# Kernel optimization log

Hardware: AMD Instinct MI355X
Metric: run time of the kernel (lower is better)

Reference implementation:

```python
import jax, jax.numpy as jnp
import numpy as np

DIM = 1024
S_SIZE = 512
M_SIZE = 4096
L_SIZE = 8192
MERGE_THRESHOLD = 0.98
L_ALPHA = 0.1
K_PROMOTE = max(1, S_SIZE // 4)  # torch: min(len(candidates), max(1, s_size//4)); candidates >> s_size here


def _l2norm(x, axis=-1):
    # F.normalize(p=2) with eps clamp
    return x / jnp.maximum(jnp.linalg.norm(x, axis=axis, keepdims=True), 1e-12)


def _update(processed_tokens, s_memory, m_memory, l_memory, m_utility, l_utility, wq, bq, wk, bk, s_ptr):
    cand = processed_tokens.reshape(-1, DIM)
    # --- S tier: scatter top-k-norm candidates into ring buffer (vectorized; K<=S so slots distinct) ---
    norms = jnp.linalg.norm(cand, axis=1)
    _, top_idx = jax.lax.top_k(norms, K_PROMOTE)
    pos = (s_ptr + jnp.arange(K_PROMOTE)) % S_SIZE
    s_mem = s_memory.at[pos].set(cand[top_idx])
    s_ptr_new = (s_ptr + K_PROMOTE) % S_SIZE
    # --- promotion attention (1 head, only attn weights used): pick best short-term slot ---
    q = l_memory.mean(axis=0) @ wq.T + bq                      # [dim]
    kproj = s_mem @ wk.T + bk                                  # [S, dim]
    attn = jax.nn.softmax(kproj @ q / jnp.sqrt(jnp.asarray(DIM, cand.dtype)))
    best_s_idx = jnp.argmax(attn)
    candidate = s_mem[best_s_idx]                              # [dim]

    # --- M tier: promote / merge / replace ---
    def not_full(mm, mu):
        ridx = jnp.argmin(mu)
        return mm.at[ridx].set(candidate), mu.at[ridx].set(mu.mean() + 1e-5)

    def full(mm, mu):
        mm_norm = _l2norm(mm)
        sims = mm_norm @ _l2norm(candidate)                    # [M]
        msi = jnp.argmax(sims)
        sim_cand = sims[msi]

        def merge_with_candidate(mm, mu):
            merged = _l2norm((mm[msi] + candidate) / 2.0)
            return mm.at[msi].set(merged), mu.at[msi].set((mu[msi] + mu.mean()) / 2.0)

        def try_internal_merge(mm, mu):
            # most redundant pair: strict lower triangle of cosine sim matrix
            sim_mat = mm_norm @ mm_norm.T                      # [M, M]
            sim_mat = jnp.where(jnp.triu(jnp.ones((M_SIZE, M_SIZE), bool)), -1.0, sim_mat)
            flat = jnp.argmax(sim_mat)
            internal_sim = sim_mat.reshape(-1)[flat]
            idx1, idx2 = flat // M_SIZE, flat % M_SIZE

            def do_pair_merge(mm, mu):
                merged = _l2norm((mm[idx1] + mm[idx2]) / 2.0)
                mm2 = mm.at[idx1].set(merged).at[idx2].set(candidate)
                mu1 = mu.at[idx1].set((mu[idx1] + mu[idx2]) / 2.0)
                mu2 = mu1.at[idx2].set(mu1.mean() + 1e-5)      # torch recomputes mean after idx1 write
                return mm2, mu2

            def replace_weakest(mm, mu):
                li = jnp.argmin(mu)
                stronger = jnp.linalg.norm(candidate) > jnp.linalg.norm(mm[li])
                mm2 = jnp.where(stronger, mm.at[li].set(candidate), mm)
                mu2 = jnp.where(stronger, mu.at[li].set(mu.mean() + 1e-5), mu)
                return mm2, mu2

            return jax.lax.cond(internal_sim > MERGE_THRESHOLD, do_pair_merge, replace_weakest, mm, mu)

        return jax.lax.cond(sim_cand > MERGE_THRESHOLD, merge_with_candidate, try_internal_merge, mm, mu)

    is_m_full = ~jnp.any(m_utility == 0)
    m_mem, m_util = jax.lax.cond(is_m_full, full, not_full, m_memory, m_utility)
    # --- L tier: consolidate most-used M slot into least-used L slot ---
    mi = jnp.argmax(m_util)
    lj = jnp.argmin(l_utility)
    consolidated = (1.0 - L_ALPHA) * l_memory[lj] + L_ALPHA * m_mem[mi]
    l_mem = l_memory.at[lj].set(consolidated)
    l_util = l_utility.at[lj].set(l_utility.mean())            # mean of pre-write values
    return s_mem, m_mem, l_mem, m_util, l_util, s_ptr_new


def setup_inputs() -> dict:
    key = jax.random.key(0)
    ks = jax.random.split(key, 10)
    scale = 1.0 / np.sqrt(DIM)
    return {
        "processed_tokens": jax.random.normal(ks[0], (4, 4096, DIM), jnp.float32),
        "s_memory": jax.random.normal(ks[1], (S_SIZE, DIM), jnp.float32),
        "m_memory": jax.random.normal(ks[2], (M_SIZE, DIM), jnp.float32),
        "l_memory": jax.random.normal(ks[3], (L_SIZE, DIM), jnp.float32),
        "m_utility": jax.random.uniform(ks[4], (M_SIZE,), jnp.float32) + 0.01,  # >0 -> 'm full' branch
        "l_utility": jax.random.uniform(ks[5], (L_SIZE,), jnp.float32) + 0.01,
        "wq": jax.random.normal(ks[6], (DIM, DIM), jnp.float32) * scale,
        "bq": jnp.zeros((DIM,), jnp.float32),
        "wk": jax.random.normal(ks[7], (DIM, DIM), jnp.float32) * scale,
        "bk": jnp.zeros((DIM,), jnp.float32),
        "s_ptr": 0,
    }


def reference(processed_tokens, s_memory, m_memory, l_memory, m_utility, l_utility, wq, bq, wk, bk, s_ptr):
    return _update(processed_tokens, s_memory, m_memory, l_memory, m_utility, l_utility, wq, bq, wk, bk, s_ptr)
```

## Files before the change

kernel.cpp:

```cpp
#include <hip/hip_runtime.h>

#define DIMV 1024
#define SSZ 512
#define MSZ 4096
#define LSZ 8192
#define KPROM 128
#define NCAND 16384
#define NPAIR 528

typedef __attribute__((ext_vector_type(4))) float f32x4;
typedef __attribute__((ext_vector_type(4))) unsigned int u32x4;
typedef __attribute__((ext_vector_type(4))) unsigned short u16x4;
typedef __attribute__((ext_vector_type(8))) __bf16 bf16x8;

#define OUT_S 0ull
#define OUT_M 524288ull
#define OUT_L 4718592ull
#define OUT_MU 13107200ull
#define OUT_LU 13111296ull
#define OUT_SPTR 13119488ull

#define SCROWS 2304
#define SC_BF16 0ull
#define SC_NORMS 2097152ull
#define SC_TOPIDX 2113536ull
#define SC_LPART 2113664ull
#define SC_RVP 2244736ull
#define SC_LOGITS 2261120ull
#define SC_BEST 2261632ull
#define SC_MNORM 2261636ull
#define SC_SIMS 2265732ull
#define SC_PPV 2269828ull
#define SC_PPI 2270356ull

__device__ __forceinline__ float wave_sum(float v) {
#pragma unroll
  for (int o = 32; o > 0; o >>= 1) v += __shfl_down(v, o, 64);
  return v;
}
__device__ __forceinline__ void wave_maxidx(float& v, int& i) {
#pragma unroll
  for (int o = 32; o > 0; o >>= 1) {
    float ov = __shfl_down(v, o, 64);
    int oi = __shfl_down(i, o, 64);
    if (ov > v || (ov == v && oi < i)) { v = ov; i = oi; }
  }
}
__device__ __forceinline__ void wave_minidx(float& v, int& i) {
#pragma unroll
  for (int o = 32; o > 0; o >>= 1) {
    float ov = __shfl_down(v, o, 64);
    int oi = __shfl_down(i, o, 64);
    if (ov < v || (ov == v && oi < i)) { v = ov; i = oi; }
  }
}
__device__ __forceinline__ unsigned short f2bf(float x) {
  unsigned u = __float_as_uint(x);
  return (unsigned short)((u + 0x7FFFu + ((u >> 16) & 1u)) >> 16);
}
__device__ __forceinline__ void gload16(const unsigned short* g, unsigned short* l) {
  __builtin_amdgcn_global_load_lds((const __attribute__((address_space(1))) unsigned int*)(g),
                                   (__attribute__((address_space(3))) unsigned int*)(l), 16, 0, 0);
}

__global__ void kA(const float* __restrict__ cand, const float* __restrict__ l_memory,
                   const float* __restrict__ m, float* __restrict__ norms,
                   float* __restrict__ lpart, unsigned short* __restrict__ mb,
                   float* __restrict__ mnorm, float* __restrict__ out_m,
                   float* __restrict__ out_l, int* __restrict__ cnt) {
  int b = blockIdx.x, t = threadIdx.x, lane = t & 63, w = t >> 6;
  if (b == 0 && t == 0) cnt[0] = 0;
  if (b < 128) {
    int r0 = b * 64;
    const f32x4* base = (const f32x4*)l_memory + (size_t)r0 * 256;
    f32x4* dst = (f32x4*)out_l + (size_t)r0 * 256;
    bool wr = (r0 >= SCROWS);
    f32x4 a0 = {0.f, 0.f, 0.f, 0.f}, a1 = a0, a2 = a0, a3 = a0;
#pragma unroll 2
    for (int r = 0; r < 64; r += 4) {
      f32x4 v0 = base[(r + 0) * 256 + t];
      f32x4 v1 = base[(r + 1) * 256 + t];
      f32x4 v2 = base[(r + 2) * 256 + t];
      f32x4 v3 = base[(r + 3) * 256 + t];
      if (wr) {
        dst[(r + 0) * 256 + t] = v0;
        dst[(r + 1) * 256 + t] = v1;
        dst[(r + 2) * 256 + t] = v2;
        dst[(r + 3) * 256 + t] = v3;
      }
      a0 += v0; a1 += v1; a2 += v2; a3 += v3;
    }
    f32x4 a = (a0 + a1) + (a2 + a3);
    ((f32x4*)(lpart + (size_t)b * DIMV))[t] = a;
  } else if (b < 384) {
    int r0 = (b - 128) * 16 + w * 4;
    const f32x4* base4 = (const f32x4*)(m + (size_t)r0 * DIMV);
    u16x4* mb4 = (u16x4*)(mb + (size_t)r0 * DIMV);
    f32x4* om4 = (f32x4*)(out_m + (size_t)r0 * DIMV);
    float s0 = 0.f, s1 = 0.f, s2 = 0.f, s3 = 0.f;
#pragma unroll
    for (int k = 0; k < 16; ++k) {
      int i = k * 64 + lane;
      f32x4 v = base4[i];
      float d = v.x * v.x + v.y * v.y + v.z * v.z + v.w * v.w;
      if (k < 4) s0 += d;
      else if (k < 8) s1 += d;
      else if (k < 12) s2 += d;
      else s3 += d;
      u16x4 h;
      h.x = f2bf(v.x); h.y = f2bf(v.y); h.z = f2bf(v.z); h.w = f2bf(v.w);
      mb4[i] = h;
      om4[i] = v;
    }
    f32x4 sv = {s0, s1, s2, s3};
#pragma unroll
    for (int o = 32; o > 0; o >>= 1) {
      sv.x += __shfl_down(sv.x, o, 64);
      sv.y += __shfl_down(sv.y, o, 64);
      sv.z += __shfl_down(sv.z, o, 64);
      sv.w += __shfl_down(sv.w, o, 64);
    }
    if (lane == 0) {
      f32x4 o4 = {sqrtf(sv.x), sqrtf(sv.y), sqrtf(sv.z), sqrtf(sv.w)};
      *((f32x4*)(mnorm + r0)) = o4;
    }
  } else {
    int r0 = (b - 384) * 16 + w * 4;
    const f32x4* base4 = (const f32x4*)(cand + (size_t)r0 * DIMV);
    float s0 = 0.f, s1 = 0.f, s2 = 0.f, s3 = 0.f;
#pragma unroll
    for (int k = 0; k < 16; ++k) {
      f32x4 v = base4[k * 64 + lane];
      float d = v.x * v.x + v.y * v.y + v.z * v.z + v.w * v.w;
      if (k < 4) s0 += d;
      else if (k < 8) s1 += d;
      else if (k < 12) s2 += d;
      else s3 += d;
    }
    f32x4 sv = {s0, s1, s2, s3};
#pragma unroll
    for (int o = 32; o > 0; o >>= 1) {
      sv.x += __shfl_down(sv.x, o, 64);
      sv.y += __shfl_down(sv.y, o, 64);
      sv.z += __shfl_down(sv.z, o, 64);
      sv.w += __shfl_down(sv.w, o, 64);
    }
    if (lane == 0) {
      f32x4 o4 = {sqrtf(sv.x), sqrtf(sv.y), sqrtf(sv.z), sqrtf(sv.w)};
      *((f32x4*)(norms + r0)) = o4;
    }
  }
}

__device__ int scan_excl_1024(int v, int* sh, int* total) {
  int t = threadIdx.x;
  sh[t] = v;
  __syncthreads();
  for (int o = 1; o < 1024; o <<= 1) {
    int x = (t >= o) ? sh[t - o] : 0;
    __syncthreads();
    sh[t] += x;
    __syncthreads();
  }
  int incl = sh[t];
  *total = sh[1023];
  __syncthreads();
  return incl - v;
}

__global__ void kT(const float* __restrict__ norms, int* __restrict__ topidx) {
  int t = threadIdx.x;
  __shared__ int sh[1024];
  __shared__ int hist[256];
  __shared__ unsigned s_selkey[KPROM];
  __shared__ int s_selidx[KPROM];
  __shared__ int s_digit, s_sub;
  unsigned key[16];
  {
    const u32x4* np = (const u32x4*)norms;
    u32x4 k0 = np[t * 4 + 0], k1 = np[t * 4 + 1], k2 = np[t * 4 + 2], k3 = np[t * 4 + 3];
    key[0] = k0.x; key[1] = k0.y; key[2] = k0.z; key[3] = k0.w;
    key[4] = k1.x; key[5] = k1.y; key[6] = k1.z; key[7] = k1.w;
    key[8] = k2.x; key[9] = k2.y; key[10] = k2.z; key[11] = k2.w;
    key[12] = k3.x; key[13] = k3.y; key[14] = k3.z; key[15] = k3.w;
  }

  unsigned prefix = 0, himask = 0;
  int remaining = KPROM;
  for (int p = 24; p >= 0; p -= 8) {
    if (t < 256) hist[t] = 0;
    __syncthreads();
#pragma unroll
    for (int j = 0; j < 16; ++j)
      if ((key[j] & himask) == prefix) atomicAdd(&hist[(key[j] >> p) & 255], 1);
    __syncthreads();
    if (t < 256) sh[t] = hist[t];
    __syncthreads();
    for (int o = 1; o < 256; o <<= 1) {
      int x = (t < 256 && t + o < 256) ? sh[t + o] : 0;
      __syncthreads();
      if (t < 256) sh[t] += x;
      __syncthreads();
    }
    if (t < 256) {
      int sfex = (t < 255) ? sh[t + 1] : 0;
      if (sfex < remaining && remaining <= sh[t]) { s_digit = t; s_sub = sfex; }
    }
    __syncthreads();
    prefix |= ((unsigned)s_digit) << p;
    remaining -= s_sub;
    himask |= (0xFFu << p);
    __syncthreads();
  }
  unsigned T = prefix;

  int cgt = 0, ceq = 0;
#pragma unroll
  for (int j = 0; j < 16; ++j) { cgt += (key[j] > T); ceq += (key[j] == T); }
  int total_gt, total_eq;
  int sgt = scan_excl_1024(cgt, sh, &total_gt);
  int seq = scan_excl_1024(ceq, sh, &total_eq);
  int need_eq = KPROM - total_gt;
  int g = sgt, e = seq;
#pragma unroll
  for (int j = 0; j < 16; ++j) {
    if (key[j] > T) { s_selkey[g] = key[j]; s_selidx[g] = t * 16 + j; ++g; }
    else if (key[j] == T) {
      if (e < need_eq) { s_selkey[total_gt + e] = key[j]; s_selidx[total_gt + e] = t * 16 + j; }
      ++e;
    }
  }
  __syncthreads();
  if (t < KPROM) {
    unsigned mk = s_selkey[t];
    int mi = s_selidx[t];
    int rank = 0;
    for (int q2 = 0; q2 < KPROM; ++q2) {
      unsigned qk = s_selkey[q2];
      int qi = s_selidx[q2];
      rank += (qk > mk || (qk == mk && qi < mi)) ? 1 : 0;
    }
    topidx[rank] = mi;
  }
}

__global__ void kBC(const float* __restrict__ cand, const float* __restrict__ s_memory,
                    const int* __restrict__ topidx, const int* __restrict__ s_ptr,
                    const float* __restrict__ wq, const float* __restrict__ bq,
                    const float* __restrict__ wk, const float* __restrict__ lpart,
                    float* __restrict__ rvpart, float* __restrict__ out_s,
                    float* __restrict__ out_sptr) {
  __shared__ float lmean_s[1024];
  __shared__ float qs[64];
  int b = blockIdx.x, t = threadIdx.x, lane = t & 63, w = t >> 6;
  if (b < 128) {
    int sp = s_ptr[0];
    if (b == 0 && t == 0) out_sptr[0] = (float)((sp + KPROM) % SSZ);
#pragma unroll
    for (int k = 0; k < 4; ++k) {
      int row = b * 4 + k;
      int ki = (row - sp + SSZ) & (SSZ - 1);
      const float* src =
          (ki < KPROM) ? (cand + (size_t)topidx[ki] * DIMV) : (s_memory + (size_t)row * DIMV);
      ((f32x4*)(out_s + (size_t)row * DIMV))[t] = ((const f32x4*)src)[t];
    }
    return;
  }
  int qb = b - 128, d0 = qb * 64;
  {
    f32x4 acc = {0.f, 0.f, 0.f, 0.f};
    for (int p = 0; p < 128; ++p) acc += ((const f32x4*)(lpart + (size_t)p * DIMV))[t];
    *(f32x4*)&lmean_s[t * 4] = acc * (1.f / 8192.f);
  }
  __syncthreads();
  for (int i = 0; i < 16; ++i) {
    int d = d0 + w * 16 + i;
    const f32x4* row = (const f32x4*)(wq + (size_t)d * DIMV);
    float s = 0.f;
#pragma unroll
    for (int c = 0; c < 4; ++c) {
      f32x4 a = row[c * 64 + lane];
      f32x4 bb = *(const f32x4*)&lmean_s[(c * 64 + lane) * 4];
      s += a.x * bb.x + a.y * bb.y + a.z * bb.z + a.w * bb.w;
    }
    s = wave_sum(s);
    if (lane == 0) qs[w * 16 + i] = s + bq[d];
  }
  __syncthreads();
  {
    f32x4 a = {0.f, 0.f, 0.f, 0.f};
    for (int r = 0; r < 64; ++r) {
      f32x4 v = ((const f32x4*)(wk + (size_t)(d0 + r) * DIMV))[t];
      a += v * qs[r];
    }
    ((f32x4*)(rvpart + (size_t)qb * DIMV))[t] = a;
  }
}

__global__ void kDE(const float* __restrict__ out_s, const float* __restrict__ rvpart,
                    float* __restrict__ logits, int* __restrict__ best,
                    float* __restrict__ cnorm, int* __restrict__ cnt) {
  __shared__ float rvs[1024];
  __shared__ float swv[4];
  __shared__ int swi[4];
  __shared__ int s_last;
  int b = blockIdx.x, t = threadIdx.x, lane = t & 63, w = t >> 6;
  {
    f32x4 acc = {0.f, 0.f, 0.f, 0.f};
#pragma unroll
    for (int p = 0; p < 16; ++p) acc += ((const f32x4*)(rvpart + (size_t)p * DIMV))[t];
    *(f32x4*)&rvs[t * 4] = acc;
  }
  __syncthreads();
  {
    int row = b * 4 + w;
    const f32x4* a4 = (const f32x4*)(out_s + (size_t)row * DIMV);
    float s = 0.f;
#pragma unroll
    for (int c = 0; c < 4; ++c) {
      f32x4 x = a4[c * 64 + lane];
      f32x4 y = *(const f32x4*)&rvs[(c * 64 + lane) * 4];
      s += x.x * y.x + x.y * y.y + x.z * y.z + x.w * y.w;
    }
    s = wave_sum(s);
    if (lane == 0) logits[row] = s;
  }
  __threadfence();
  __syncthreads();
  if (t == 0) {
    int a = __hip_atomic_fetch_add(cnt, 1, __ATOMIC_ACQ_REL, __HIP_MEMORY_SCOPE_AGENT);
    s_last = (a == 127) ? 1 : 0;
  }
  __syncthreads();
  if (!s_last) return;
  __threadfence();
  {
    float v0 = logits[t], v1 = logits[t + 256];
    float bv;
    int bidx;
    if (v1 > v0) { bv = v1; bidx = t + 256; } else { bv = v0; bidx = t; }
    wave_maxidx(bv, bidx);
    if (lane == 0) { swv[w] = bv; swi[w] = bidx; }
    __syncthreads();
    if (t == 0) {
      float a = swv[0]; int ai = swi[0];
      for (int i = 1; i < 4; ++i)
        if (swv[i] > a || (swv[i] == a && swi[i] < ai)) { a = swv[i]; ai = swi[i]; }
      best[0] = ai;
      cnt[0] = 0;
    }
    __syncthreads();
    int bi = best[0];
    f32x4 c4 = ((const f32x4*)(out_s + (size_t)bi * DIMV))[t];
    float s = c4.x * c4.x + c4.y * c4.y + c4.z * c4.z + c4.w * c4.w;
    s = wave_sum(s);
    __syncthreads();
    if (lane == 0) swv[w] = s;
    __syncthreads();
    if (t == 0) cnorm[0] = sqrtf(swv[0] + swv[1] + swv[2] + swv[3]);
  }
}

__global__ __launch_bounds__(256, 3) void kG(const unsigned short* __restrict__ mb,
                                             const float* __restrict__ mnorm,
                                             const float* __restrict__ m,
                                             const float* __restrict__ out_s,
                                             const int* __restrict__ best,
                                             const float* __restrict__ cnorm,
                                             float* __restrict__ pv, int* __restrict__ pidx,
                                             float* __restrict__ sims) {
  int b = blockIdx.x, t = threadIdx.x, lane = t & 63, w = t >> 6;
  if (b >= NPAIR) {
    int row = (b - NPAIR) * 4 + w;
    const f32x4* mp = (const f32x4*)(m + (size_t)row * DIMV);
    const f32x4* cp = (const f32x4*)(out_s + (size_t)best[0] * DIMV);
    float sd = 0.f;
#pragma unroll
    for (int c = 0; c < 4; ++c) {
      int i = c * 64 + lane;
      f32x4 v = mp[i], u = cp[i];
      sd += v.x * u.x + v.y * u.y + v.z * u.z + v.w * u.w;
    }
    sd = wave_sum(sd);
    if (lane == 0) sims[row] = sd / (fmaxf(mnorm[row], 1e-12f) * fmaxf(cnorm[0], 1e-12f));
    return;
  }
  __shared__ unsigned short Ash[128 * 64];
  __shared__ unsigned short Bsh[128 * 64];
  __shared__ float spv[4];
  __shared__ int spi[4];

  int bs = (b & 7) * 66 + (b >> 3);
  int bi = (int)((sqrtf(8.f * (float)bs + 1.f) - 1.f) * 0.5f);
  while (bi * (bi + 1) / 2 > bs) --bi;
  while ((bi + 1) * (bi + 2) / 2 <= bs) ++bi;
  int bj = bs - bi * (bi + 1) / 2;
  int rowA0 = bi * 128, rowB0 = bj * 128;

  int wr = w >> 1, wc = w & 1;
  int rl = lane & 15, kq4 = lane >> 4;
  int swz = rl & 7;
  int subrow = lane >> 3, gg = lane & 7;
  int gsw = (gg ^ subrow) << 3;

  f32x4 acc[4][4];
  f32x4 z = {0.f, 0.f, 0.f, 0.f};
#pragma unroll
  for (int ti = 0; ti < 4; ++ti)
#pragma unroll
    for (int tj = 0; tj < 4; ++tj) acc[ti][tj] = z;

  for (int kc = 0; kc < DIMV; kc += 64) {
#pragma unroll
    for (int jj = 0; jj < 4; ++jj) {
      int rsub = w * 32 + jj * 8 + subrow;
      gload16(mb + (size_t)(rowA0 + rsub) * DIMV + kc + gsw, Ash + (w * 4 + jj) * 512);
      gload16(mb + (size_t)(rowB0 + rsub) * DIMV + kc + gsw, Bsh + (w * 4 + jj) * 512);
    }
    __syncthreads();
#pragma unroll
    for (int ks = 0; ks < 2; ++ks) {
      int co = (((ks * 4 + kq4) ^ swz) << 3);
      bf16x8 af[4], bfv[4];
#pragma unroll
      for (int ti = 0; ti < 4; ++ti)
        af[ti] = *(const bf16x8*)(Ash + (wr * 64 + ti * 16 + rl) * 64 + co);
#pragma unroll
      for (int tj = 0; tj < 4; ++tj)
        bfv[tj] = *(const bf16x8*)(Bsh + (wc * 64 + tj * 16 + rl) * 64 + co);
#pragma unroll
      for (int ti = 0; ti < 4; ++ti)
#pragma unroll
        for (int tj = 0; tj < 4; ++tj)
          acc[ti][tj] = __builtin_amdgcn_mfma_f32_16x16x32_bf16(af[ti], bfv[tj], acc[ti][tj], 0, 0, 0);
    }
    __syncthreads();
  }

  float ni[16], nj4[4];
#pragma unroll
  for (int ti = 0; ti < 4; ++ti)
#pragma unroll
    for (int r = 0; r < 4; ++r)
      ni[ti * 4 + r] = fmaxf(mnorm[rowA0 + wr * 64 + ti * 16 + kq4 * 4 + r], 1e-12f);
#pragma unroll
  for (int tj = 0; tj < 4; ++tj)
    nj4[tj] = fmaxf(mnorm[rowB0 + wc * 64 + tj * 16 + rl], 1e-12f);

  float bv = -3.402823466e38f;
  int bidx = 0x7FFFFFFF;
#pragma unroll
  for (int ti = 0; ti < 4; ++ti)
#pragma unroll
    for (int tj = 0; tj < 4; ++tj)
#pragma unroll
      for (int r = 0; r < 4; ++r) {
        int gi = rowA0 + wr * 64 + ti * 16 + kq4 * 4 + r;
        int gj = rowB0 + wc * 64 + tj * 16 + rl;
        if (gi > gj) {
          float s = acc[ti][tj][r] / (ni[ti * 4 + r] * nj4[tj]);
          int fi = gi * MSZ + gj;
          if (s > bv || (s == bv && fi < bidx)) { bv = s; bidx = fi; }
        }
      }
  wave_maxidx(bv, bidx);
  if (lane == 0) { spv[w] = bv; spi[w] = bidx; }
  __syncthreads();
  if (t == 0) {
    float a = spv[0]; int ai = spi[0];
    for (int i = 1; i < 4; ++i)
      if (spv[i] > a || (spv[i] == a && spi[i] < ai)) { a = spv[i]; ai = spi[i]; }
    pv[b] = a;
    pidx[b] = ai;
  }
}

__global__ void kH(const float* __restrict__ pv, const int* __restrict__ pidx,
                   const float* __restrict__ sims, const float* __restrict__ mu,
                   const float* __restrict__ mnorm, const float* __restrict__ cnorm,
                   const int* __restrict__ best, const float* __restrict__ lu,
                   const float* __restrict__ m, const float* __restrict__ l_memory,
                   const float* __restrict__ out_s, float* __restrict__ out_mu,
                   float* __restrict__ out_lu, float* __restrict__ out_m,
                   float* __restrict__ out_l, int* __restrict__ ws) {
  __shared__ float swv[16];
  __shared__ int swi[16];
  __shared__ float ssum[16];
  __shared__ int szf[16];
  __shared__ float s_res[2];
  __shared__ int s_resi[2];
  __shared__ int s_branch, s_i1, s_i2, s_lj, s_best, s_mi;
  __shared__ float s_u1, s_u2, s_lmean, s_nrm;
  int t = threadIdx.x, lane = t & 63, w = t >> 6;

  float bv = -3.402823466e38f;
  int bidx = 0x7FFFFFFF;
  for (int i = t; i < NPAIR; i += 1024) {
    float v = pv[i];
    int fi = pidx[i];
    if (v > bv || (v == bv && fi < bidx)) { bv = v; bidx = fi; }
  }
  wave_maxidx(bv, bidx);
  if (lane == 0) { swv[w] = bv; swi[w] = bidx; }
  __syncthreads();
  if (t == 0) {
    float a = swv[0]; int ai = swi[0];
    for (int i = 1; i < 16; ++i)
      if (swv[i] > a || (swv[i] == a && swi[i] < ai)) { a = swv[i]; ai = swi[i]; }
    s_res[0] = a; s_resi[0] = ai;
  }
  __syncthreads();

  bv = -3.402823466e38f;
  bidx = 0x7FFFFFFF;
#pragma unroll
  for (int j = 0; j < 4; ++j) {
    int i = t * 4 + j;
    float v = sims[i];
    if (v > bv) { bv = v; bidx = i; }
  }
  wave_maxidx(bv, bidx);
  if (lane == 0) { swv[w] = bv; swi[w] = bidx; }
  __syncthreads();
  if (t == 0) {
    float a = swv[0]; int ai = swi[0];
    for (int i = 1; i < 16; ++i)
      if (swv[i] > a || (swv[i] == a && swi[i] < ai)) { a = swv[i]; ai = swi[i]; }
    s_res[1] = a; s_resi[1] = ai;
  }
  __syncthreads();

  float muv[4];
  float sum = 0.f, mnv = 3.402823466e38f;
  int mni = 0x7FFFFFFF, zf = 0;
#pragma unroll
  for (int j = 0; j < 4; ++j) {
    int i = t * 4 + j;
    float v = mu[i];
    muv[j] = v;
    sum += v;
    if (v < mnv) { mnv = v; mni = i; }
    if (v == 0.f) zf = 1;
  }
  sum = wave_sum(sum);
  wave_minidx(mnv, mni);
#pragma unroll
  for (int o = 32; o > 0; o >>= 1) zf |= __shfl_down(zf, o, 64);
  if (lane == 0) { ssum[w] = sum; swv[w] = mnv; swi[w] = mni; szf[w] = zf; }
  __syncthreads();
  if (t == 0) {
    float muSum = 0.f;
    int anyz = 0;
    float a = swv[0]; int li = swi[0];
    for (int i = 0; i < 16; ++i) {
      muSum += ssum[i];
      anyz |= szf[i];
      if (i > 0 && (swv[i] < a || (swv[i] == a && swi[i] < li))) { a = swv[i]; li = swi[i]; }
    }
    float muMean = muSum / 4096.f;
    float internal_sim = s_res[0];
    int iflat = s_resi[0];
    float sim_cand = s_res[1];
    int msi = s_resi[1];
    int branch, i1 = -1, i2 = -1;
    float u1 = 0.f, u2 = 0.f;
    if (anyz) {
      branch = 0; i1 = li; u1 = muMean + 1e-5f;
    } else if (sim_cand > 0.98f) {
      branch = 1; i1 = msi; u1 = (mu[msi] + muMean) * 0.5f;
    } else if (internal_sim > 0.98f) {
      branch = 2; i1 = iflat / MSZ; i2 = iflat - (iflat / MSZ) * MSZ;
      float o1 = mu[i1], o2 = mu[i2];
      u1 = (o1 + o2) * 0.5f;
      u2 = (muSum - o1 + u1) / 4096.f + 1e-5f;
    } else {
      if (cnorm[0] > mnorm[li]) { branch = 0; i1 = li; u1 = muMean + 1e-5f; }
      else branch = 4;
    }
    s_branch = branch; s_i1 = i1; s_i2 = i2; s_u1 = u1; s_u2 = u2;
    s_best = best[0];
    ws[2] = branch; ws[3] = i1; ws[4] = i2; ws[5] = best[0];
  }
  __syncthreads();

  int branch = s_branch, i1 = s_i1, i2 = s_i2;
  float u1 = s_u1, u2 = s_u2;
  bv = -3.402823466e38f;
  bidx = 0x7FFFFFFF;
#pragma unroll
  for (int j = 0; j < 4; ++j) {
    int i = t * 4 + j;
    float v = muv[j];
    if (branch != 4 && i == i1) v = u1;
    if (branch == 2 && i == i2) v = u2;
    out_mu[i] = v;
    if (v > bv) { bv = v; bidx = i; }
  }
  wave_maxidx(bv, bidx);
  __syncthreads();
  if (lane == 0) { swv[w] = bv; swi[w] = bidx; }
  __syncthreads();
  if (t == 0) {
    float a = swv[0]; int ai = swi[0];
    for (int i = 1; i < 16; ++i)
      if (swv[i] > a || (swv[i] == a && swi[i] < ai)) { a = swv[i]; ai = swi[i]; }
    ws[1] = ai;
    s_mi = ai;
  }

  float luv[8];
  sum = 0.f; mnv = 3.402823466e38f; mni = 0x7FFFFFFF;
#pragma unroll
  for (int j = 0; j < 8; ++j) {
    int i = t * 8 + j;
    float v = lu[i];
    luv[j] = v;
    sum += v;
    if (v < mnv) { mnv = v; mni = i; }
  }
  sum = wave_sum(sum);
  wave_minidx(mnv, mni);
  __syncthreads();
  if (lane == 0) { swv[w] = mnv; swi[w] = mni; ssum[w] = sum; }
  __syncthreads();
  if (t == 0) {
    float a = swv[0]; int ai = swi[0];
    float ls = 0.f;
    for (int i = 0; i < 16; ++i) {
      ls += ssum[i];
      if (i > 0 && (swv[i] < a || (swv[i] == a && swi[i] < ai))) { a = swv[i]; ai = swi[i]; }
    }
    s_lj = ai;
    s_lmean = ls / 8192.f;
    ws[0] = ai;
  }
  __syncthreads();
  {
    int lj = s_lj;
    float lmv = s_lmean;
#pragma unroll
    for (int j = 0; j < 8; ++j) {
      int i = t * 8 + j;
      out_lu[i] = (i == lj) ? lmv : luv[j];
    }
  }
  __syncthreads();

  int fbest = s_best, fmi = s_mi, flj = s_lj;
  const f32x4* csrc = (const f32x4*)(out_s + (size_t)fbest * DIMV);
  {
    f32x4 v = {0.f, 0.f, 0.f, 0.f};
    float ssv = 0.f;
    if (t < 256 && branch != 4 && branch != 0) {
      f32x4 a = ((const f32x4*)(m + (size_t)i1 * DIMV))[t];
      f32x4 bb = (branch == 1) ? csrc[t] : ((const f32x4*)(m + (size_t)i2 * DIMV))[t];
      v = (a + bb) * 0.5f;
      ssv = v.x * v.x + v.y * v.y + v.z * v.z + v.w * v.w;
    }
    ssv = wave_sum(ssv);
    __syncthreads();
    if (lane == 0) ssum[w] = ssv;
    __syncthreads();
    if (t == 0) {
      float s2 = 0.f;
      for (int i = 0; i < 16; ++i) s2 += ssum[i];
      s_nrm = fmaxf(sqrtf(s2), 1e-12f);
    }
    __syncthreads();
    if (t < 256 && branch != 4) {
      f32x4* dst = (f32x4*)(out_m + (size_t)i1 * DIMV);
      dst[t] = (branch == 0) ? csrc[t] : (v / s_nrm);
      if (branch == 2) ((f32x4*)(out_m + (size_t)i2 * DIMV))[t] = csrc[t];
    }
  }
  __syncthreads();

  {
    int mode = 0;
    if ((branch == 0 && fmi == i1) || (branch == 2 && fmi == i2)) mode = 1;
    else if (branch == 1 && fmi == i1) mode = 2;
    else if (branch == 2 && fmi == i1) mode = 3;
    f32x4 vm = {0.f, 0.f, 0.f, 0.f};
    float ssv = 0.f;
    if (t < 256 && (mode == 2 || mode == 3)) {
      f32x4 a = ((const f32x4*)(m + (size_t)fmi * DIMV))[t];
      f32x4 bb = (mode == 2) ? csrc[t] : ((const f32x4*)(m + (size_t)i2 * DIMV))[t];
      vm = (a + bb) * 0.5f;
      ssv = vm.x * vm.x + vm.y * vm.y + vm.z * vm.z + vm.w * vm.w;
    }
    ssv = wave_sum(ssv);
    __syncthreads();
    if (lane == 0) ssum[w] = ssv;
    __syncthreads();
    if (t == 0) {
      float s2 = 0.f;
      for (int i = 0; i < 16; ++i) s2 += ssum[i];
      s_nrm = fmaxf(sqrtf(s2), 1e-12f);
    }
    __syncthreads();
    if (t < 256) {
      f32x4 lv = ((const f32x4*)(l_memory + (size_t)flj * DIMV))[t];
      f32x4 mv;
      if (mode == 0) mv = ((const f32x4*)(m + (size_t)fmi * DIMV))[t];
      else if (mode == 1) mv = csrc[t];
      else mv = vm / s_nrm;
      ((f32x4*)(out_l + (size_t)flj * DIMV))[t] = lv * 0.9f + mv * 0.1f;
    }
  }
}

__global__ void kI(const float* __restrict__ l_memory, const int* __restrict__ ws,
                   float* __restrict__ out_l) {
  int b = blockIdx.x, t = threadIdx.x;
  int lj = ws[0];
  int r0 = b * 4;
  const f32x4* src = (const f32x4*)(l_memory + (size_t)r0 * DIMV);
  f32x4* dst = (f32x4*)(out_l + (size_t)r0 * DIMV);
#pragma unroll
  for (int k = 0; k < 4; ++k) {
    if (r0 + k == lj) continue;
    dst[k * 256 + t] = src[k * 256 + t];
  }
}

extern "C" void kernel_launch(void* const* d_in, const int* in_sizes, int n_in,
                              void* d_out, int out_size, void* d_ws, size_t ws_size,
                              hipStream_t stream) {
  const float* cand = (const float*)d_in[0];
  const float* s_memory = (const float*)d_in[1];
  const float* m_memory = (const float*)d_in[2];
  const float* l_memory = (const float*)d_in[3];
  const float* m_utility = (const float*)d_in[4];
  const float* l_utility = (const float*)d_in[5];
  const float* wq = (const float*)d_in[6];
  const float* bq = (const float*)d_in[7];
  const float* wk = (const float*)d_in[8];
  const float* bk = (const float*)d_in[9];
  const int* s_ptr = (const int*)d_in[10];
  (void)bk;

  float* out = (float*)d_out;
  float* out_s = out + OUT_S;
  float* out_m = out + OUT_M;
  float* out_l = out + OUT_L;
  float* out_mu = out + OUT_MU;
  float* out_lu = out + OUT_LU;
  float* out_sptr = out + OUT_SPTR;

  float* lsc = out_l;
  unsigned short* mb = (unsigned short*)(lsc + SC_BF16);
  float* norms = lsc + SC_NORMS;
  int* topidx = (int*)(lsc + SC_TOPIDX);
  float* lpart = lsc + SC_LPART;
  float* rvpart = lsc + SC_RVP;
  float* logits = lsc + SC_LOGITS;
  int* best = (int*)(lsc + SC_BEST);
  float* cnorm = lsc + SC_BEST + 1;
  float* mnorm = lsc + SC_MNORM;
  float* sims = lsc + SC_SIMS;
  float* pv = lsc + SC_PPV;
  int* pidx = (int*)(lsc + SC_PPI);
  int* wsctl = (int*)d_ws;

  kA<<<1408, 256, 0, stream>>>(cand, l_memory, m_memory, norms, lpart, mb, mnorm, out_m, out_l,
                               wsctl + 8);
  kT<<<1, 1024, 0, stream>>>(norms, topidx);
  kBC<<<144, 256, 0, stream>>>(cand, s_memory, topidx, s_ptr, wq, bq, wk, lpart, rvpart, out_s,
                               out_sptr);
  kDE<<<128, 256, 0, stream>>>(out_s, rvpart, logits, best, cnorm, wsctl + 8);
  kG<<<NPAIR + 1024, 256, 0, stream>>>(mb, mnorm, m_memory, out_s, best, cnorm, pv, pidx, sims);
  kH<<<1, 1024, 0, stream>>>(pv, pidx, sims, m_utility, mnorm, cnorm, best, l_utility, m_memory,
                             l_memory, out_s, out_mu, out_lu, out_m, out_l, wsctl);
  kI<<<576, 256, 0, stream>>>(l_memory, wsctl, out_l);
}
```

Baseline: 309.7 us.

## Defer M and L passthrough copies to final kernel and use per-wave histograms

Result: faster. 301.7 us (-2.6%).

```diff
diff --git a/kernel.cpp b/kernel.cpp
--- a/kernel.cpp
+++ b/kernel.cpp
@@ -20,7 +20,6 @@
 #define OUT_LU 13111296ull
 #define OUT_SPTR 13119488ull
 
-#define SCROWS 2304
 #define SC_BF16 0ull
 #define SC_NORMS 2097152ull
 #define SC_TOPIDX 2113536ull
@@ -66,29 +65,19 @@
 __global__ void kA(const float* __restrict__ cand, const float* __restrict__ l_memory,
                    const float* __restrict__ m, float* __restrict__ norms,
                    float* __restrict__ lpart, unsigned short* __restrict__ mb,
-                   float* __restrict__ mnorm, float* __restrict__ out_m,
-                   float* __restrict__ out_l, int* __restrict__ cnt) {
+                   float* __restrict__ mnorm, int* __restrict__ cnt) {
   int b = blockIdx.x, t = threadIdx.x, lane = t & 63, w = t >> 6;
   if (b == 0 && t == 0) cnt[0] = 0;
   if (b < 128) {
     int r0 = b * 64;
     const f32x4* base = (const f32x4*)l_memory + (size_t)r0 * 256;
-    f32x4* dst = (f32x4*)out_l + (size_t)r0 * 256;
-    bool wr = (r0 >= SCROWS);
     f32x4 a0 = {0.f, 0.f, 0.f, 0.f}, a1 = a0, a2 = a0, a3 = a0;
 #pragma unroll 2
     for (int r = 0; r < 64; r += 4) {
-      f32x4 v0 = base[(r + 0) * 256 + t];
-      f32x4 v1 = base[(r + 1) * 256 + t];
-      f32x4 v2 = base[(r + 2) * 256 + t];
-      f32x4 v3 = base[(r + 3) * 256 + t];
-      if (wr) {
-        dst[(r + 0) * 256 + t] = v0;
-        dst[(r + 1) * 256 + t] = v1;
-        dst[(r + 2) * 256 + t] = v2;
-        dst[(r + 3) * 256 + t] = v3;
-      }
-      a0 += v0; a1 += v1; a2 += v2; a3 += v3;
+      a0 += base[(r + 0) * 256 + t];
+      a1 += base[(r + 1) * 256 + t];
+      a2 += base[(r + 2) * 256 + t];
+      a3 += base[(r + 3) * 256 + t];
     }
     f32x4 a = (a0 + a1) + (a2 + a3);
     ((f32x4*)(lpart + (size_t)b * DIMV))[t] = a;
@@ -96,7 +85,6 @@
     int r0 = (b - 128) * 16 + w * 4;
     const f32x4* base4 = (const f32x4*)(m + (size_t)r0 * DIMV);
     u16x4* mb4 = (u16x4*)(mb + (size_t)r0 * DIMV);
-    f32x4* om4 = (f32x4*)(out_m + (size_t)r0 * DIMV);
     float s0 = 0.f, s1 = 0.f, s2 = 0.f, s3 = 0.f;
 #pragma unroll
     for (int k = 0; k < 16; ++k) {
@@ -110,7 +98,6 @@
       u16x4 h;
       h.x = f2bf(v.x); h.y = f2bf(v.y); h.z = f2bf(v.z); h.w = f2bf(v.w);
       mb4[i] = h;
-      om4[i] = v;
     }
     f32x4 sv = {s0, s1, s2, s3};
 #pragma unroll
@@ -169,9 +156,9 @@
 }
 
 __global__ void kT(const float* __restrict__ norms, int* __restrict__ topidx) {
-  int t = threadIdx.x;
+  int t = threadIdx.x, w = t >> 6;
   __shared__ int sh[1024];
-  __shared__ int hist[256];
+  __shared__ int histW[16][256];
   __shared__ unsigned s_selkey[KPROM];
   __shared__ int s_selidx[KPROM];
   __shared__ int s_digit, s_sub;
@@ -188,13 +175,19 @@
   unsigned prefix = 0, himask = 0;
   int remaining = KPROM;
   for (int p = 24; p >= 0; p -= 8) {
-    if (t < 256) hist[t] = 0;
+#pragma unroll
+    for (int i = 0; i < 4; ++i) ((int*)histW)[t + i * 1024] = 0;
     __syncthreads();
 #pragma unroll
     for (int j = 0; j < 16; ++j)
-      if ((key[j] & himask) == prefix) atomicAdd(&hist[(key[j] >> p) & 255], 1);
-    __syncthreads();
-    if (t < 256) sh[t] = hist[t];
+      if ((key[j] & himask) == prefix) atomicAdd(&histW[w][(key[j] >> p) & 255], 1);
+    __syncthreads();
+    if (t < 256) {
+      int h = 0;
+#pragma unroll
+      for (int w2 = 0; w2 < 16; ++w2) h += histW[w2][t];
+      sh[t] = h;
+    }
     __syncthreads();
     for (int o = 1; o < 256; o <<= 1) {
       int x = (t < 256 && t + o < 256) ? sh[t + o] : 0;
@@ -709,17 +702,30 @@
   }
 }
 
-__global__ void kI(const float* __restrict__ l_memory, const int* __restrict__ ws,
+__global__ void kI(const float* __restrict__ m, const float* __restrict__ l_memory,
+                   const int* __restrict__ ws, float* __restrict__ out_m,
                    float* __restrict__ out_l) {
   int b = blockIdx.x, t = threadIdx.x;
-  int lj = ws[0];
-  int r0 = b * 4;
-  const f32x4* src = (const f32x4*)(l_memory + (size_t)r0 * DIMV);
-  f32x4* dst = (f32x4*)(out_l + (size_t)r0 * DIMV);
-#pragma unroll
-  for (int k = 0; k < 4; ++k) {
-    if (r0 + k == lj) continue;
-    dst[k * 256 + t] = src[k * 256 + t];
+  int lj = ws[0], branch = ws[2], i1 = ws[3], i2 = ws[4];
+  if (b < 1024) {
+    int r0 = b * 4;
+    const f32x4* src = (const f32x4*)(m + (size_t)r0 * DIMV);
+    f32x4* dst = (f32x4*)(out_m + (size_t)r0 * DIMV);
+#pragma unroll
+    for (int k = 0; k < 4; ++k) {
+      int row = r0 + k;
+      if ((branch != 4 && row == i1) || (branch == 2 && row == i2)) continue;
+      dst[k * 256 + t] = src[k * 256 + t];
+    }
+  } else {
+    int r0 = (b - 1024) * 4;
+    const f32x4* src = (const f32x4*)(l_memory + (size_t)r0 * DIMV);
+    f32x4* dst = (f32x4*)(out_l + (size_t)r0 * DIMV);
+#pragma unroll
+    for (int k = 0; k < 4; ++k) {
+      if (r0 + k == lj) continue;
+      dst[k * 256 + t] = src[k * 256 + t];
+    }
   }
 }
 
@@ -762,8 +768,7 @@
   int* pidx = (int*)(lsc + SC_PPI);
   int* wsctl = (int*)d_ws;
 
-  kA<<<1408, 256, 0, stream>>>(cand, l_memory, m_memory, norms, lpart, mb, mnorm, out_m, out_l,
-                               wsctl + 8);
+  kA<<<1408, 256, 0, stream>>>(cand, l_memory, m_memory, norms, lpart, mb, mnorm, wsctl + 8);
   kT<<<1, 1024, 0, stream>>>(norms, topidx);
   kBC<<<144, 256, 0, stream>>>(cand, s_memory, topidx, s_ptr, wq, bq, wk, lpart, rvpart, out_s,
                                out_sptr);
@@ -771,5 +776,5 @@
   kG<<<NPAIR + 1024, 256, 0, stream>>>(mb, mnorm, m_memory, out_s, best, cnorm, pv, pidx, sims);
   kH<<<1, 1024, 0, stream>>>(pv, pidx, sims, m_utility, mnorm, cnorm, best, l_utility, m_memory,
                              l_memory, out_s, out_mu, out_lu, out_m, out_l, wsctl);
-  kI<<<576, 256, 0, stream>>>(l_memory, wsctl, out_l);
-}
+  kI<<<3072, 256, 0, stream>>>(m_memory, l_memory, wsctl, out_m, out_l);
+}
```

## Split query/key projection into wider kernels and privatize top-k histograms per wave

Applied to the files above, without the earlier changes.

After: 294.0 us. 5.1% less time.

```diff
diff --git a/kernel.cpp b/kernel.cpp
--- a/kernel.cpp
+++ b/kernel.cpp
@@ -25,13 +25,15 @@
 #define SC_NORMS 2097152ull
 #define SC_TOPIDX 2113536ull
 #define SC_LPART 2113664ull
-#define SC_RVP 2244736ull
-#define SC_LOGITS 2261120ull
-#define SC_BEST 2261632ull
-#define SC_MNORM 2261636ull
-#define SC_SIMS 2265732ull
-#define SC_PPV 2269828ull
-#define SC_PPI 2270356ull
+#define SC_RV 2244736ull
+#define SC_LMEAN 2245760ull
+#define SC_QV 2246784ull
+#define SC_LOGITS 2247808ull
+#define SC_BEST 2248320ull
+#define SC_MNORM 2248336ull
+#define SC_SIMS 2252432ull
+#define SC_PPV 2256528ull
+#define SC_PPI 2257056ull
 
 __device__ __forceinline__ float wave_sum(float v) {
 #pragma unroll
@@ -168,33 +170,46 @@
   return incl - v;
 }
 
-__global__ void kT(const float* __restrict__ norms, int* __restrict__ topidx) {
+__global__ void kT(const float* __restrict__ norms, int* __restrict__ topidx,
+                   const float* __restrict__ lpart, float* __restrict__ lmean) {
   int t = threadIdx.x;
+  if (blockIdx.x == 1) {
+    float s0 = 0.f, s1 = 0.f, s2 = 0.f, s3 = 0.f;
+    for (int p = 0; p < 128; p += 4) {
+      s0 += lpart[(size_t)(p + 0) * DIMV + t];
+      s1 += lpart[(size_t)(p + 1) * DIMV + t];
+      s2 += lpart[(size_t)(p + 2) * DIMV + t];
+      s3 += lpart[(size_t)(p + 3) * DIMV + t];
+    }
+    lmean[t] = ((s0 + s1) + (s2 + s3)) * (1.f / 8192.f);
+    return;
+  }
+  int w = t >> 6;
   __shared__ int sh[1024];
-  __shared__ int hist[256];
+  __shared__ int histW[16][256];
   __shared__ unsigned s_selkey[KPROM];
   __shared__ int s_selidx[KPROM];
   __shared__ int s_digit, s_sub;
   unsigned key[16];
-  {
-    const u32x4* np = (const u32x4*)norms;
-    u32x4 k0 = np[t * 4 + 0], k1 = np[t * 4 + 1], k2 = np[t * 4 + 2], k3 = np[t * 4 + 3];
-    key[0] = k0.x; key[1] = k0.y; key[2] = k0.z; key[3] = k0.w;
-    key[4] = k1.x; key[5] = k1.y; key[6] = k1.z; key[7] = k1.w;
-    key[8] = k2.x; key[9] = k2.y; key[10] = k2.z; key[11] = k2.w;
-    key[12] = k3.x; key[13] = k3.y; key[14] = k3.z; key[15] = k3.w;
-  }
+#pragma unroll
+  for (int j = 0; j < 16; ++j) key[j] = __float_as_uint(norms[t * 16 + j]);
 
   unsigned prefix = 0, himask = 0;
   int remaining = KPROM;
   for (int p = 24; p >= 0; p -= 8) {
-    if (t < 256) hist[t] = 0;
+#pragma unroll
+    for (int i = 0; i < 4; ++i) ((int*)histW)[t + i * 1024] = 0;
     __syncthreads();
 #pragma unroll
     for (int j = 0; j < 16; ++j)
-      if ((key[j] & himask) == prefix) atomicAdd(&hist[(key[j] >> p) & 255], 1);
-    __syncthreads();
-    if (t < 256) sh[t] = hist[t];
+      if ((key[j] & himask) == prefix) atomicAdd(&histW[w][(key[j] >> p) & 255], 1);
+    __syncthreads();
+    if (t < 256) {
+      int h = 0;
+#pragma unroll
+      for (int w2 = 0; w2 < 16; ++w2) h += histW[w2][t];
+      sh[t] = h;
+    }
     __syncthreads();
     for (int o = 1; o < 256; o <<= 1) {
       int x = (t < 256 && t + o < 256) ? sh[t + o] : 0;
@@ -244,82 +259,69 @@
   }
 }
 
-__global__ void kBC(const float* __restrict__ cand, const float* __restrict__ s_memory,
-                    const int* __restrict__ topidx, const int* __restrict__ s_ptr,
-                    const float* __restrict__ wq, const float* __restrict__ bq,
-                    const float* __restrict__ wk, const float* __restrict__ lpart,
-                    float* __restrict__ rvpart, float* __restrict__ out_s,
-                    float* __restrict__ out_sptr) {
-  __shared__ float lmean_s[1024];
-  __shared__ float qs[64];
-  int b = blockIdx.x, t = threadIdx.x, lane = t & 63, w = t >> 6;
-  if (b < 128) {
+__global__ void kB(const float* __restrict__ cand, const float* __restrict__ s_memory,
+                   const int* __restrict__ topidx, const int* __restrict__ s_ptr,
+                   const float* __restrict__ wq, const float* __restrict__ bq,
+                   const float* __restrict__ lmean, float* __restrict__ out_s,
+                   float* __restrict__ out_sptr, float* __restrict__ qv,
+                   float* __restrict__ rv) {
+  int b = blockIdx.x, t = threadIdx.x;
+  if (b < 512) {
     int sp = s_ptr[0];
+    int k = (b - sp + SSZ) & (SSZ - 1);
+    const float* src = (k < KPROM) ? (cand + (size_t)topidx[k] * DIMV) : (s_memory + (size_t)b * DIMV);
+    ((f32x4*)(out_s + (size_t)b * DIMV))[t] = ((const f32x4*)src)[t];
     if (b == 0 && t == 0) out_sptr[0] = (float)((sp + KPROM) % SSZ);
-#pragma unroll
-    for (int k = 0; k < 4; ++k) {
-      int row = b * 4 + k;
-      int ki = (row - sp + SSZ) & (SSZ - 1);
-      const float* src =
-          (ki < KPROM) ? (cand + (size_t)topidx[ki] * DIMV) : (s_memory + (size_t)row * DIMV);
-      ((f32x4*)(out_s + (size_t)row * DIMV))[t] = ((const f32x4*)src)[t];
-    }
-    return;
-  }
-  int qb = b - 128, d0 = qb * 64;
-  {
-    f32x4 acc = {0.f, 0.f, 0.f, 0.f};
-    for (int p = 0; p < 128; ++p) acc += ((const f32x4*)(lpart + (size_t)p * DIMV))[t];
-    *(f32x4*)&lmean_s[t * 4] = acc * (1.f / 8192.f);
-  }
-  __syncthreads();
-  for (int i = 0; i < 16; ++i) {
-    int d = d0 + w * 16 + i;
+  } else {
+    if (b == 512) {
+      f32x4 z = {0.f, 0.f, 0.f, 0.f};
+      ((f32x4*)rv)[t] = z;
+    }
+    int lane = t & 63, w = t >> 6;
+    int d = (b - 512) * 4 + w;
     const f32x4* row = (const f32x4*)(wq + (size_t)d * DIMV);
+    const f32x4* lm = (const f32x4*)lmean;
     float s = 0.f;
 #pragma unroll
     for (int c = 0; c < 4; ++c) {
-      f32x4 a = row[c * 64 + lane];
-      f32x4 bb = *(const f32x4*)&lmean_s[(c * 64 + lane) * 4];
+      f32x4 a = row[c * 64 + lane], bb = lm[c * 64 + lane];
       s += a.x * bb.x + a.y * bb.y + a.z * bb.z + a.w * bb.w;
     }
     s = wave_sum(s);
-    if (lane == 0) qs[w * 16 + i] = s + bq[d];
-  }
-  __syncthreads();
-  {
-    f32x4 a = {0.f, 0.f, 0.f, 0.f};
-    for (int r = 0; r < 64; ++r) {
-      f32x4 v = ((const f32x4*)(wk + (size_t)(d0 + r) * DIMV))[t];
-      a += v * qs[r];
-    }
-    ((f32x4*)(rvpart + (size_t)qb * DIMV))[t] = a;
-  }
-}
-
-__global__ void kDE(const float* __restrict__ out_s, const float* __restrict__ rvpart,
+    if (lane == 0) qv[d] = s + bq[d];
+  }
+}
+
+__global__ void kC(const float* __restrict__ wk, const float* __restrict__ qv,
+                   float* __restrict__ rv) {
+  int b = blockIdx.x, t = threadIdx.x;
+  f32x4 a = {0.f, 0.f, 0.f, 0.f};
+  for (int r = 0; r < 8; ++r) {
+    float qd = qv[b * 8 + r];
+    f32x4 v = ((const f32x4*)(wk + (size_t)(b * 8 + r) * DIMV))[t];
+    a += v * qd;
+  }
+  atomicAdd(&rv[t * 4 + 0], a.x);
+  atomicAdd(&rv[t * 4 + 1], a.y);
+  atomicAdd(&rv[t * 4 + 2], a.z);
+  atomicAdd(&rv[t * 4 + 3], a.w);
+}
+
+__global__ void kDE(const float* __restrict__ out_s, const float* __restrict__ rv,
                     float* __restrict__ logits, int* __restrict__ best,
                     float* __restrict__ cnorm, int* __restrict__ cnt) {
-  __shared__ float rvs[1024];
   __shared__ float swv[4];
   __shared__ int swi[4];
   __shared__ int s_last;
   int b = blockIdx.x, t = threadIdx.x, lane = t & 63, w = t >> 6;
   {
-    f32x4 acc = {0.f, 0.f, 0.f, 0.f};
-#pragma unroll
-    for (int p = 0; p < 16; ++p) acc += ((const f32x4*)(rvpart + (size_t)p * DIMV))[t];
-    *(f32x4*)&rvs[t * 4] = acc;
-  }
-  __syncthreads();
-  {
     int row = b * 4 + w;
     const f32x4* a4 = (const f32x4*)(out_s + (size_t)row * DIMV);
+    const f32x4* r4 = (const f32x4*)rv;
     float s = 0.f;
 #pragma unroll
     for (int c = 0; c < 4; ++c) {
-      f32x4 x = a4[c * 64 + lane];
-      f32x4 y = *(const f32x4*)&rvs[(c * 64 + lane) * 4];
+      f32x4 x = a4[c * 64 + lane], y = r4[c * 64 + lane];
       s += x.x * y.x + x.y * y.y + x.z * y.z + x.w * y.w;
     }
     s = wave_sum(s);
@@ -752,7 +754,9 @@
   float* norms = lsc + SC_NORMS;
   int* topidx = (int*)(lsc + SC_TOPIDX);
   float* lpart = lsc + SC_LPART;
-  float* rvpart = lsc + SC_RVP;
+  float* rv = lsc + SC_RV;
+  float* lmean = lsc + SC_LMEAN;
+  float* qv = lsc + SC_QV;
   float* logits = lsc + SC_LOGITS;
   int* best = (int*)(lsc + SC_BEST);
   float* cnorm = lsc + SC_BEST + 1;
@@ -764,10 +768,11 @@
 
   kA<<<1408, 256, 0, stream>>>(cand, l_memory, m_memory, norms, lpart, mb, mnorm, out_m, out_l,
                                wsctl + 8);
-  kT<<<1, 1024, 0, stream>>>(norms, topidx);
-  kBC<<<144, 256, 0, stream>>>(cand, s_memory, topidx, s_ptr, wq, bq, wk, lpart, rvpart, out_s,
-                               out_sptr);
-  kDE<<<128, 256, 0, stream>>>(out_s, rvpart, logits, best, cnorm, wsctl + 8);
+  kT<<<2, 1024, 0, stream>>>(norms, topidx, lpart, lmean);
+  kB<<<768, 256, 0, stream>>>(cand, s_memory, topidx, s_ptr, wq, bq, lmean, out_s, out_sptr, qv,
+                              rv);
+  kC<<<128, 256, 0, stream>>>(wk, qv, rv);
+  kDE<<<128, 256, 0, stream>>>(out_s, rv, logits, best, cnorm, wsctl + 8);
   kG<<<NPAIR + 1024, 256, 0, stream>>>(mb, mnorm, m_memory, out_s, best, cnorm, pv, pidx, sims);
   kH<<<1, 1024, 0, stream>>>(pv, pidx, sims, m_utility, mnorm, cnorm, best, l_utility, m_memory,
                              l_memory, out_s, out_mu, out_lu, out_m, out_l, wsctl);
```
